# Kernel tuning notes

Hardware: AMD Instinct MI355X
Metric: run time of the kernel (lower is better)

Reference implementation:

```python
import jax, jax.numpy as jnp
import numpy as np

VOCAB, E, H = 32000, 512, 512
B, T = 256, 128
EPS = 1e-12  # F.normalize eps


def setup_inputs() -> dict:
    key = jax.random.key(0)
    ks = jax.random.split(key, 9)
    s_e = 1.0 / np.sqrt(E)
    s_h = 1.0 / np.sqrt(H)
    captions = jax.random.randint(ks[0], (B, T), 0, VOCAB, dtype=jnp.int32)
    emb = jax.random.normal(ks[1], (VOCAB, E), dtype=jnp.float32)
    # fused input->gates weight [E,4H] (gate order: i, f, o, g) and bias [4H]
    Wx = jax.random.uniform(ks[2], (E, 4 * H), jnp.float32, -s_e, s_e)
    bx = jax.random.uniform(ks[3], (4 * H,), jnp.float32, -s_e, s_e)
    # fused hidden->gates weight [H,4H] and bias [4H]
    Uh = jax.random.uniform(ks[4], (H, 4 * H), jnp.float32, -s_h, s_h)
    bu = jax.random.uniform(ks[5], (4 * H,), jnp.float32, -s_h, s_h)
    fcW = jax.random.uniform(ks[6], (H, E), jnp.float32, -s_h, s_h)
    fcb = jax.random.uniform(ks[7], (E,), jnp.float32, -s_h, s_h)
    return {"captions": captions, "emb": emb, "Wx": Wx, "bx": bx,
            "Uh": Uh, "bu": bu, "fcW": fcW, "fcb": fcb}


def reference(captions, emb, Wx, bx, Uh, bu, fcW, fcb):
    # padding_idx=0: embedding row 0 is zero
    emb = emb.at[0].set(0.0)
    x = emb[captions]  # [B,T,E]
    # precompute all input-to-gate projections in one fused GEMM
    xg = jnp.einsum('bte,ef->btf', x, Wx) + bx  # [B,T,4H]

    def step(carry, xg_t):
        h, c = carry
        g = xg_t + h @ Uh + bu  # [B,4H]
        i, f, o, gg = jnp.split(g, 4, axis=-1)
        c = jax.nn.sigmoid(f) * c + jax.nn.sigmoid(i) * jnp.tanh(gg)
        h = jax.nn.sigmoid(o) * jnp.tanh(c)
        return (h, c), None

    h0 = jnp.zeros((captions.shape[0], H), xg.dtype)
    (h, _), _ = jax.lax.scan(step, (h0, h0), jnp.swapaxes(xg, 0, 1))
    out = h @ fcW + fcb  # [B,E]
    norm = jnp.sqrt(jnp.sum(out * out, axis=1, keepdims=True))
    return out / jnp.maximum(norm, EPS)
```

## Files before the change

kernel.cpp:

```cpp
#include <hip/hip_runtime.h>

#define B_ 256
#define T_ 128
#define E_ 512
#define H_ 512
#define NG 2048
#define NB 256
#define NT 512

typedef __attribute__((ext_vector_type(8))) short bf16x8;
typedef __attribute__((ext_vector_type(4))) float f32x4;
typedef unsigned long long u64;

__device__ __forceinline__ short f2bf(float f) {
  union { float f; unsigned u; } x; x.f = f;
  unsigned r = x.u + 0x7FFFu + ((x.u >> 16) & 1u);
  return (short)(r >> 16);
}
__device__ __forceinline__ float bf2f(short s) {
  union { unsigned u; float f; } x;
  x.u = ((unsigned)(unsigned short)s) << 16; return x.f;
}
__device__ __forceinline__ float sigm(float x) { return 1.0f / (1.0f + __expf(-x)); }
__device__ __forceinline__ float tanh_(float x) {
  float cx = fminf(fmaxf(x, -9.f), 9.f);
  float e = __expf(2.f * cx);
  return (e - 1.f) / (e + 1.f);
}

__global__ __launch_bounds__(256) void prep_w(const float* __restrict__ Wx,
                                              const float* __restrict__ Uh,
                                              short* __restrict__ Wt) {
  __shared__ float tile[64][65];
  const int k0 = blockIdx.x * 64;
  const int j0 = blockIdx.y * 64;
  const int tx = threadIdx.x & 63, ty = threadIdx.x >> 6;
#pragma unroll
  for (int r = 0; r < 16; ++r) {
    int k = k0 + r * 4 + ty;
    float v = (k < 512) ? Wx[(size_t)k * NG + j0 + tx]
                        : Uh[(size_t)(k - 512) * NG + j0 + tx];
    tile[r * 4 + ty][tx] = v;
  }
  __syncthreads();
#pragma unroll
  for (int r = 0; r < 16; ++r) {
    int j = j0 + r * 4 + ty;
    Wt[(size_t)j * 1024 + k0 + tx] = f2bf(tile[tx][r * 4 + ty]);
  }
}

__global__ __launch_bounds__(256) void stage_x(const int* __restrict__ captions,
                                               const float* __restrict__ emb,
                                               short* __restrict__ xs) {
  const int bid = blockIdx.x;
  const int t = bid >> 8, b = bid & 255;
  const int tok = captions[b * T_ + t];
  short* o = xs + (size_t)bid * E_;
  const float* src = emb + (size_t)tok * E_;
  int e0 = threadIdx.x, e1 = threadIdx.x + 256;
  if (tok) { o[e0] = f2bf(src[e0]); o[e1] = f2bf(src[e1]); }
  else     { o[e0] = 0;             o[e1] = 0; }
}

__global__ __launch_bounds__(NT, 2) void lstm_all(
    const short* __restrict__ xs,
    const short* __restrict__ Wt,
    const float* __restrict__ bx, const float* __restrict__ bu,
    unsigned* __restrict__ hb0, unsigned* __restrict__ hb1,
    unsigned* __restrict__ flags) {
  __shared__ float part[2][3][2][4][16][20];

  const int tid = threadIdx.x;
  const int wid = tid >> 6, lane = tid & 63;
  const int l15 = lane & 15, l4 = lane >> 4;
  const int kq = wid >> 1, mh = wid & 1;
  const int mg = blockIdx.x >> 5, jt = blockIdx.x & 31;
  const int j0 = jt * 16;
  const int rA = mg * 32 + mh * 16 + l15;

  bf16x8 bfr[4][8];
#pragma unroll
  for (int g = 0; g < 4; ++g) {
    const short* wp = Wt + (size_t)(g * 512 + j0 + l15) * 1024 + kq * 256 + l4 * 8;
#pragma unroll
    for (int ks = 0; ks < 8; ++ks)
      bfr[g][ks] = *(const bf16x8*)(wp + ks * 32);
  }
#pragma unroll
  for (int g = 0; g < 4; ++g)
#pragma unroll
    for (int ks = 0; ks < 8; ++ks)
      asm volatile("" : "+v"(bfr[g][ks]));

  const int J = j0 + l15;
  const float bi  = bx[J] + bu[J];
  const float bf_ = bx[512 + J] + bu[512 + J];
  const float bo  = bx[1024 + J] + bu[1024 + J];
  const float bg  = bx[1536 + J] + bu[1536 + J];
  float c_reg[4] = {0.f, 0.f, 0.f, 0.f};

  unsigned* fl = flags + mg * 64 * 32;

  for (int t = 0; t < T_; ++t) {
    const int tp = t & 1;
    unsigned* hout = tp ? hb1 : hb0;
    const unsigned* hin = tp ? hb0 : hb1;

    f32x4 acc[4] = {{0,0,0,0},{0,0,0,0},{0,0,0,0},{0,0,0,0}};

    if (kq < 2) {
      const short* ab = xs + ((size_t)t * B_ + rA) * E_ + kq * 256 + l4 * 8;
      bf16x8 af[8];
#pragma unroll
      for (int ks = 0; ks < 8; ++ks) af[ks] = *(const bf16x8*)(ab + ks * 32);
#pragma unroll
      for (int ks = 0; ks < 8; ++ks)
#pragma unroll
        for (int g = 0; g < 4; ++g)
          acc[g] = __builtin_amdgcn_mfma_f32_16x16x32_bf16(af[ks], bfr[g][ks], acc[g], 0, 0, 0);
    } else if (t > 0) {
      const unsigned* myfl = fl + (mh * 32 + (kq - 2) * 16 + l15) * 32;
      unsigned v = __hip_atomic_load(myfl, __ATOMIC_RELAXED, __HIP_MEMORY_SCOPE_AGENT);
      while (!__all((int)(v >= (unsigned)t))) {
        __builtin_amdgcn_s_sleep(1);
        v = __hip_atomic_load(myfl, __ATOMIC_RELAXED, __HIP_MEMORY_SCOPE_AGENT);
      }
      asm volatile("" ::: "memory");
      const u64* hp = (const u64*)hin + (size_t)rA * 128 + (kq - 2) * 64 + l4 * 2;
      u64 w[16];
#pragma unroll
      for (int ks = 0; ks < 8; ++ks) {
        w[ks * 2]     = __hip_atomic_load(hp + ks * 8,     __ATOMIC_RELAXED, __HIP_MEMORY_SCOPE_AGENT);
        w[ks * 2 + 1] = __hip_atomic_load(hp + ks * 8 + 1, __ATOMIC_RELAXED, __HIP_MEMORY_SCOPE_AGENT);
      }
#pragma unroll
      for (int ks = 0; ks < 8; ++ks) {
        union { bf16x8 v; unsigned u[4]; } fa;
        fa.u[0] = (unsigned)w[ks * 2];
        fa.u[1] = (unsigned)(w[ks * 2] >> 32);
        fa.u[2] = (unsigned)w[ks * 2 + 1];
        fa.u[3] = (unsigned)(w[ks * 2 + 1] >> 32);
#pragma unroll
        for (int g = 0; g < 4; ++g)
          acc[g] = __builtin_amdgcn_mfma_f32_16x16x32_bf16(fa.v, bfr[g][ks], acc[g], 0, 0, 0);
      }
    }

    if (kq != 2) {
      const int slot = (kq == 3) ? 2 : kq;
#pragma unroll
      for (int g = 0; g < 4; ++g)
#pragma unroll
        for (int r = 0; r < 4; ++r)
          part[tp][slot][mh][g][l4 * 4 + r][l15] = acc[g][r];
    }
    asm volatile("s_waitcnt lgkmcnt(0)" ::: "memory");
    __builtin_amdgcn_s_barrier();

    if (kq == 2) {
#pragma unroll
      for (int g = 0; g < 4; ++g)
#pragma unroll
        for (int r = 0; r < 4; ++r)
          acc[g][r] += part[tp][0][mh][g][l4 * 4 + r][l15]
                     + part[tp][1][mh][g][l4 * 4 + r][l15]
                     + part[tp][2][mh][g][l4 * 4 + r][l15];
      unsigned hw[4];
#pragma unroll
      for (int r = 0; r < 4; ++r) {
        float iv = acc[0][r] + bi, fv = acc[1][r] + bf_;
        float ov = acc[2][r] + bo, gv = acc[3][r] + bg;
        float cn = sigm(fv) * c_reg[r] + sigm(iv) * tanh_(gv);
        c_reg[r] = cn;
        hw[r] = (unsigned)(unsigned short)f2bf(sigm(ov) * tanh_(cn));
      }
#pragma unroll
      for (int r = 0; r < 4; ++r) {
        unsigned other = (unsigned)__shfl_xor((int)hw[r], 1, 64);
        if (!(l15 & 1)) {
          const int R = mg * 32 + mh * 16 + l4 * 4 + r;
          __hip_atomic_store(hout + (size_t)R * 256 + (J >> 1),
                             hw[r] | (other << 16),
                             __ATOMIC_RELAXED, __HIP_MEMORY_SCOPE_AGENT);
        }
      }
      asm volatile("s_waitcnt vmcnt(0)" ::: "memory");
      if (lane == 0)
        __hip_atomic_store(fl + (mh * 32 + jt) * 32, (unsigned)(t + 1),
                           __ATOMIC_RELAXED, __HIP_MEMORY_SCOPE_AGENT);
    }
  }
}

__global__ __launch_bounds__(256) void final_fc(const unsigned* __restrict__ h,
                                                const float* __restrict__ fcW,
                                                const float* __restrict__ fcb,
                                                float* __restrict__ out) {
  const int b = blockIdx.x, tid = threadIdx.x;
  __shared__ float hrow[512];
  __shared__ float red[256];
  {
    unsigned w = h[(size_t)b * 256 + tid];
    hrow[tid * 2]     = bf2f((short)(w & 0xFFFF));
    hrow[tid * 2 + 1] = bf2f((short)(w >> 16));
  }
  __syncthreads();
  float a0 = fcb[tid], a1 = fcb[tid + 256];
  for (int k = 0; k < 512; ++k) {
    float hv = hrow[k];
    a0 += hv * fcW[(size_t)k * 512 + tid];
    a1 += hv * fcW[(size_t)k * 512 + tid + 256];
  }
  red[tid] = a0 * a0 + a1 * a1;
  __syncthreads();
  for (int s = 128; s > 0; s >>= 1) {
    if (tid < s) red[tid] += red[tid + s];
    __syncthreads();
  }
  float scale = 1.0f / fmaxf(sqrtf(red[0]), 1e-12f);
  out[(size_t)b * 512 + tid] = a0 * scale;
  out[(size_t)b * 512 + tid + 256] = a1 * scale;
}

extern "C" void kernel_launch(void* const* d_in, const int* in_sizes, int n_in,
                              void* d_out, int out_size, void* d_ws, size_t ws_size,
                              hipStream_t stream) {
  const int*   captions = (const int*)d_in[0];
  const float* emb      = (const float*)d_in[1];
  const float* Wx       = (const float*)d_in[2];
  const float* bx       = (const float*)d_in[3];
  const float* Uh       = (const float*)d_in[4];
  const float* bu       = (const float*)d_in[5];
  const float* fcW      = (const float*)d_in[6];
  const float* fcb      = (const float*)d_in[7];
  float* out = (float*)d_out;

  char* ws = (char*)d_ws;
  size_t off = 0;
  auto alloc = [&](size_t bytes) {
    char* p = ws + off;
    off += (bytes + 255) & ~(size_t)255;
    return p;
  };
  short*    Wt    = (short*)alloc((size_t)NG * 1024 * 2);
  short*    xs    = (short*)alloc((size_t)T_ * B_ * E_ * 2);
  unsigned* hb0   = (unsigned*)alloc((size_t)B_ * 256 * 4);
  unsigned* hb1   = (unsigned*)alloc((size_t)B_ * 256 * 4);
  unsigned* flags = (unsigned*)alloc(8 * 64 * 32 * 4);

  hipMemsetAsync(flags, 0, 8 * 64 * 32 * 4, stream);

  prep_w<<<dim3(16, 32), 256, 0, stream>>>(Wx, Uh, Wt);
  stage_x<<<T_ * B_, 256, 0, stream>>>(captions, emb, xs);

  void* kargs[] = {(void*)&xs, (void*)&Wt, (void*)&bx, (void*)&bu,
                   (void*)&hb0, (void*)&hb1, (void*)&flags};
  hipLaunchCooperativeKernel((const void*)lstm_all, dim3(NB), dim3(NT),
                             kargs, 0, stream);

  final_fc<<<B_, 256, 0, stream>>>(hb1, fcW, fcb, out);
}
```

Before: 695.0 us.

## Split recurrent h wait into halves and vectorize LDS partial-sum exchange

The recurrent-path waves now wait only on the flags of the producers of the first half of the K range, run those MFMAs, and then wait for the rest. This overlaps part of the cross-block synchronisation with compute. The spin loop backs off to longer sleeps after a few tries, and the shared-memory partial sums become f32x4 stores and loads in place of scalar accesses. The risks are finer-grained polling overhead, added wake-up latency from the longer sleep, and possible LDS bank conflicts now that the padding is gone.

```diff
diff --git a/kernel.cpp b/kernel.cpp
--- a/kernel.cpp
+++ b/kernel.cpp
@@ -69,7 +69,7 @@
     const float* __restrict__ bx, const float* __restrict__ bu,
     unsigned* __restrict__ hb0, unsigned* __restrict__ hb1,
     unsigned* __restrict__ flags) {
-  __shared__ float part[2][3][2][4][16][20];
+  __shared__ f32x4 part[2][3][2][4][4][16];
 
   const int tid = threadIdx.x;
   const int wid = tid >> 6, lane = tid & 63;
@@ -120,22 +120,25 @@
         for (int g = 0; g < 4; ++g)
           acc[g] = __builtin_amdgcn_mfma_f32_16x16x32_bf16(af[ks], bfr[g][ks], acc[g], 0, 0, 0);
     } else if (t > 0) {
+      const unsigned thr = (unsigned)t;
       const unsigned* myfl = fl + (mh * 32 + (kq - 2) * 16 + l15) * 32;
+      const u64* hp = (const u64*)hin + (size_t)rA * 128 + (kq - 2) * 64 + l4 * 2;
       unsigned v = __hip_atomic_load(myfl, __ATOMIC_RELAXED, __HIP_MEMORY_SCOPE_AGENT);
-      while (!__all((int)(v >= (unsigned)t))) {
-        __builtin_amdgcn_s_sleep(1);
+      int spin = 0;
+      while (!__all((int)((l15 >= 8) | (v >= thr)))) {
+        if (spin++ < 4) __builtin_amdgcn_s_sleep(1);
+        else            __builtin_amdgcn_s_sleep(8);
         v = __hip_atomic_load(myfl, __ATOMIC_RELAXED, __HIP_MEMORY_SCOPE_AGENT);
       }
       asm volatile("" ::: "memory");
-      const u64* hp = (const u64*)hin + (size_t)rA * 128 + (kq - 2) * 64 + l4 * 2;
       u64 w[16];
 #pragma unroll
-      for (int ks = 0; ks < 8; ++ks) {
+      for (int ks = 0; ks < 4; ++ks) {
         w[ks * 2]     = __hip_atomic_load(hp + ks * 8,     __ATOMIC_RELAXED, __HIP_MEMORY_SCOPE_AGENT);
         w[ks * 2 + 1] = __hip_atomic_load(hp + ks * 8 + 1, __ATOMIC_RELAXED, __HIP_MEMORY_SCOPE_AGENT);
       }
 #pragma unroll
-      for (int ks = 0; ks < 8; ++ks) {
+      for (int ks = 0; ks < 4; ++ks) {
         union { bf16x8 v; unsigned u[4]; } fa;
         fa.u[0] = (unsigned)w[ks * 2];
         fa.u[1] = (unsigned)(w[ks * 2] >> 32);
@@ -145,15 +148,35 @@
         for (int g = 0; g < 4; ++g)
           acc[g] = __builtin_amdgcn_mfma_f32_16x16x32_bf16(fa.v, bfr[g][ks], acc[g], 0, 0, 0);
       }
+      while (!__all((int)(v >= thr))) {
+        if (spin++ < 4) __builtin_amdgcn_s_sleep(1);
+        else            __builtin_amdgcn_s_sleep(8);
+        v = __hip_atomic_load(myfl, __ATOMIC_RELAXED, __HIP_MEMORY_SCOPE_AGENT);
+      }
+      asm volatile("" ::: "memory");
+#pragma unroll
+      for (int ks = 4; ks < 8; ++ks) {
+        w[ks * 2]     = __hip_atomic_load(hp + ks * 8,     __ATOMIC_RELAXED, __HIP_MEMORY_SCOPE_AGENT);
+        w[ks * 2 + 1] = __hip_atomic_load(hp + ks * 8 + 1, __ATOMIC_RELAXED, __HIP_MEMORY_SCOPE_AGENT);
+      }
+#pragma unroll
+      for (int ks = 4; ks < 8; ++ks) {
+        union { bf16x8 v; unsigned u[4]; } fa;
+        fa.u[0] = (unsigned)w[ks * 2];
+        fa.u[1] = (unsigned)(w[ks * 2] >> 32);
+        fa.u[2] = (unsigned)w[ks * 2 + 1];
+        fa.u[3] = (unsigned)(w[ks * 2 + 1] >> 32);
+#pragma unroll
+        for (int g = 0; g < 4; ++g)
+          acc[g] = __builtin_amdgcn_mfma_f32_16x16x32_bf16(fa.v, bfr[g][ks], acc[g], 0, 0, 0);
+      }
     }
 
     if (kq != 2) {
       const int slot = (kq == 3) ? 2 : kq;
 #pragma unroll
       for (int g = 0; g < 4; ++g)
-#pragma unroll
-        for (int r = 0; r < 4; ++r)
-          part[tp][slot][mh][g][l4 * 4 + r][l15] = acc[g][r];
+        part[tp][slot][mh][g][l4][l15] = acc[g];
     }
     asm volatile("s_waitcnt lgkmcnt(0)" ::: "memory");
     __builtin_amdgcn_s_barrier();
@@ -161,11 +184,9 @@
     if (kq == 2) {
 #pragma unroll
       for (int g = 0; g < 4; ++g)
-#pragma unroll
-        for (int r = 0; r < 4; ++r)
-          acc[g][r] += part[tp][0][mh][g][l4 * 4 + r][l15]
-                     + part[tp][1][mh][g][l4 * 4 + r][l15]
-                     + part[tp][2][mh][g][l4 * 4 + r][l15];
+        acc[g] += part[tp][0][mh][g][l4][l15]
+                + part[tp][1][mh][g][l4][l15]
+                + part[tp][2][mh][g][l4][l15];
       unsigned hw[4];
 #pragma unroll
       for (int r = 0; r < 4; ++r) {
```

Measured after the change: 694.6 us. Within noise of the previous version (-0.1%).

## Split gate reduction and cell update across input-side waves, add per-publisher flags

Applied to the files above, without the earlier changes.

The cross-wave reduction of gate partial sums and the LSTM cell update move from the two h-side waves to the two x-side waves (kq<2). Each wave now finishes 2 rows instead of 4, and all four waves write f32x4 partials to shared memory. Flags are split per (kq, mh) publisher, and consumers poll the matching publisher flags. The spin-wait also backs off to a longer sleep after a few tries. The intent is to take the nonlinear update off the h-path waves so they can start polling for the next step sooner, and to spread the elementwise work wider. The cost is extra shared-memory traffic and longer sleeps, which can add wake-up latency.

```diff
diff --git a/kernel.cpp b/kernel.cpp
--- a/kernel.cpp
+++ b/kernel.cpp
@@ -69,7 +69,7 @@
     const float* __restrict__ bx, const float* __restrict__ bu,
     unsigned* __restrict__ hb0, unsigned* __restrict__ hb1,
     unsigned* __restrict__ flags) {
-  __shared__ float part[2][3][2][4][16][20];
+  __shared__ f32x4 part[2][4][2][4][4][16];
 
   const int tid = threadIdx.x;
   const int wid = tid >> 6, lane = tid & 63;
@@ -98,9 +98,9 @@
   const float bf_ = bx[512 + J] + bu[512 + J];
   const float bo  = bx[1024 + J] + bu[1024 + J];
   const float bg  = bx[1536 + J] + bu[1536 + J];
-  float c_reg[4] = {0.f, 0.f, 0.f, 0.f};
-
-  unsigned* fl = flags + mg * 64 * 32;
+  float c_reg[2] = {0.f, 0.f};
+
+  unsigned* fl = flags + mg * 4 * 32 * 32;
 
   for (int t = 0; t < T_; ++t) {
     const int tp = t & 1;
@@ -120,10 +120,15 @@
         for (int g = 0; g < 4; ++g)
           acc[g] = __builtin_amdgcn_mfma_f32_16x16x32_bf16(af[ks], bfr[g][ks], acc[g], 0, 0, 0);
     } else if (t > 0) {
-      const unsigned* myfl = fl + (mh * 32 + (kq - 2) * 16 + l15) * 32;
+      const unsigned thr = (unsigned)t;
+      const int jtp = (lane & 15) + (kq - 2) * 16;
+      const int pub = ((lane >> 4) & 1) * 2 + mh;
+      const unsigned* myfl = fl + (pub * 32 + jtp) * 32;
       unsigned v = __hip_atomic_load(myfl, __ATOMIC_RELAXED, __HIP_MEMORY_SCOPE_AGENT);
-      while (!__all((int)(v >= (unsigned)t))) {
-        __builtin_amdgcn_s_sleep(1);
+      int spin = 0;
+      while (!__all((int)(v >= thr))) {
+        if (spin++ < 4) __builtin_amdgcn_s_sleep(1);
+        else            __builtin_amdgcn_s_sleep(8);
         v = __hip_atomic_load(myfl, __ATOMIC_RELAXED, __HIP_MEMORY_SCOPE_AGENT);
       }
       asm volatile("" ::: "memory");
@@ -147,39 +152,36 @@
       }
     }
 
-    if (kq != 2) {
-      const int slot = (kq == 3) ? 2 : kq;
-#pragma unroll
-      for (int g = 0; g < 4; ++g)
-#pragma unroll
-        for (int r = 0; r < 4; ++r)
-          part[tp][slot][mh][g][l4 * 4 + r][l15] = acc[g][r];
-    }
+#pragma unroll
+    for (int g = 0; g < 4; ++g)
+      part[tp][kq][mh][g][l4][l15] = acc[g];
     asm volatile("s_waitcnt lgkmcnt(0)" ::: "memory");
     __builtin_amdgcn_s_barrier();
 
-    if (kq == 2) {
-#pragma unroll
-      for (int g = 0; g < 4; ++g)
-#pragma unroll
-        for (int r = 0; r < 4; ++r)
-          acc[g][r] += part[tp][0][mh][g][l4 * 4 + r][l15]
-                     + part[tp][1][mh][g][l4 * 4 + r][l15]
-                     + part[tp][2][mh][g][l4 * 4 + r][l15];
-      unsigned hw[4];
-#pragma unroll
-      for (int r = 0; r < 4; ++r) {
-        float iv = acc[0][r] + bi, fv = acc[1][r] + bf_;
-        float ov = acc[2][r] + bo, gv = acc[3][r] + bg;
+    if (kq < 2) {
+      unsigned hw[2];
+#pragma unroll
+      for (int r = 0; r < 2; ++r) {
+        const int Rm = kq * 8 + l4 * 2 + r;
+        const int ri = Rm >> 2, rc = Rm & 3;
+        float sums[4];
+#pragma unroll
+        for (int g = 0; g < 4; ++g)
+          sums[g] = part[tp][0][mh][g][ri][l15][rc]
+                  + part[tp][1][mh][g][ri][l15][rc]
+                  + part[tp][2][mh][g][ri][l15][rc]
+                  + part[tp][3][mh][g][ri][l15][rc];
+        float iv = sums[0] + bi, fv = sums[1] + bf_;
+        float ov = sums[2] + bo, gv = sums[3] + bg;
         float cn = sigm(fv) * c_reg[r] + sigm(iv) * tanh_(gv);
         c_reg[r] = cn;
         hw[r] = (unsigned)(unsigned short)f2bf(sigm(ov) * tanh_(cn));
       }
 #pragma unroll
-      for (int r = 0; r < 4; ++r) {
+      for (int r = 0; r < 2; ++r) {
         unsigned other = (unsigned)__shfl_xor((int)hw[r], 1, 64);
         if (!(l15 & 1)) {
-          const int R = mg * 32 + mh * 16 + l4 * 4 + r;
+          const int R = mg * 32 + mh * 16 + kq * 8 + l4 * 2 + r;
           __hip_atomic_store(hout + (size_t)R * 256 + (J >> 1),
                              hw[r] | (other << 16),
                              __ATOMIC_RELAXED, __HIP_MEMORY_SCOPE_AGENT);
@@ -187,7 +189,7 @@
       }
       asm volatile("s_waitcnt vmcnt(0)" ::: "memory");
       if (lane == 0)
-        __hip_atomic_store(fl + (mh * 32 + jt) * 32, (unsigned)(t + 1),
+        __hip_atomic_store(fl + ((kq * 2 + mh) * 32 + jt) * 32, (unsigned)(t + 1),
                            __ATOMIC_RELAXED, __HIP_MEMORY_SCOPE_AGENT);
     }
   }
@@ -247,9 +249,9 @@
   short*    xs    = (short*)alloc((size_t)T_ * B_ * E_ * 2);
   unsigned* hb0   = (unsigned*)alloc((size_t)B_ * 256 * 4);
   unsigned* hb1   = (unsigned*)alloc((size_t)B_ * 256 * 4);
-  unsigned* flags = (unsigned*)alloc(8 * 64 * 32 * 4);
-
-  hipMemsetAsync(flags, 0, 8 * 64 * 32 * 4, stream);
+  unsigned* flags = (unsigned*)alloc(8 * 4 * 32 * 32 * 4);
+
+  hipMemsetAsync(flags, 0, 8 * 4 * 32 * 32 * 4, stream);
 
   prep_w<<<dim3(16, 32), 256, 0, stream>>>(Wx, Uh, Wt);
   stage_x<<<T_ * B_, 256, 0, stream>>>(captions, emb, xs);
```

New measurement: 753.9 us. +8.5%, slower.

## Repartition LSTM blocks into 16-row batch groups with 32 hidden columns each

Applied to the files above, without the earlier changes.

Changes the cooperative LSTM decomposition from 8 batch groups of 32 rows by 32 column tiles to 16 batch groups of 16 rows by 16 column tiles of 32 hidden units. Each block's two wave halves now split hidden columns instead of batch rows. A block therefore waits on flags from only 16 other blocks per group rather than 32, which shrinks the cross-block synchronisation fan-in each step. It also stores partial sums as f32x4 vectors in shared memory and adds a backoff to the spin-wait sleep, which may add latency when the wait runs long.

```diff
diff --git a/kernel.cpp b/kernel.cpp
--- a/kernel.cpp
+++ b/kernel.cpp
@@ -69,20 +69,21 @@
     const float* __restrict__ bx, const float* __restrict__ bu,
     unsigned* __restrict__ hb0, unsigned* __restrict__ hb1,
     unsigned* __restrict__ flags) {
-  __shared__ float part[2][3][2][4][16][20];
+  __shared__ f32x4 part[2][3][2][4][4][16];
 
   const int tid = threadIdx.x;
   const int wid = tid >> 6, lane = tid & 63;
   const int l15 = lane & 15, l4 = lane >> 4;
-  const int kq = wid >> 1, mh = wid & 1;
-  const int mg = blockIdx.x >> 5, jt = blockIdx.x & 31;
-  const int j0 = jt * 16;
-  const int rA = mg * 32 + mh * 16 + l15;
+  const int kq = wid >> 1, jh = wid & 1;
+  const int mg = blockIdx.x >> 4, jt = blockIdx.x & 15;
+  const int j0 = jt * 32;
+  const int rA = mg * 16 + l15;
 
   bf16x8 bfr[4][8];
 #pragma unroll
   for (int g = 0; g < 4; ++g) {
-    const short* wp = Wt + (size_t)(g * 512 + j0 + l15) * 1024 + kq * 256 + l4 * 8;
+    const short* wp = Wt + (size_t)(g * 512 + j0 + jh * 16 + l15) * 1024
+                         + kq * 256 + l4 * 8;
 #pragma unroll
     for (int ks = 0; ks < 8; ++ks)
       bfr[g][ks] = *(const bf16x8*)(wp + ks * 32);
@@ -93,14 +94,14 @@
     for (int ks = 0; ks < 8; ++ks)
       asm volatile("" : "+v"(bfr[g][ks]));
 
-  const int J = j0 + l15;
+  const int J = j0 + jh * 16 + l15;
   const float bi  = bx[J] + bu[J];
   const float bf_ = bx[512 + J] + bu[512 + J];
   const float bo  = bx[1024 + J] + bu[1024 + J];
   const float bg  = bx[1536 + J] + bu[1536 + J];
   float c_reg[4] = {0.f, 0.f, 0.f, 0.f};
 
-  unsigned* fl = flags + mg * 64 * 32;
+  unsigned* fl = flags + mg * 1024;
 
   for (int t = 0; t < T_; ++t) {
     const int tp = t & 1;
@@ -120,10 +121,15 @@
         for (int g = 0; g < 4; ++g)
           acc[g] = __builtin_amdgcn_mfma_f32_16x16x32_bf16(af[ks], bfr[g][ks], acc[g], 0, 0, 0);
     } else if (t > 0) {
-      const unsigned* myfl = fl + (mh * 32 + (kq - 2) * 16 + l15) * 32;
+      const unsigned thr = (unsigned)t;
+      const int jtp = (kq - 2) * 8 + (lane >> 1 & 7);
+      const int jhp = lane & 1;
+      const unsigned* myfl = fl + (jhp * 16 + jtp) * 32;
       unsigned v = __hip_atomic_load(myfl, __ATOMIC_RELAXED, __HIP_MEMORY_SCOPE_AGENT);
-      while (!__all((int)(v >= (unsigned)t))) {
-        __builtin_amdgcn_s_sleep(1);
+      int spin = 0;
+      while (!__all((int)((lane >= 16) | (v >= thr)))) {
+        if (spin++ < 4) __builtin_amdgcn_s_sleep(1);
+        else            __builtin_amdgcn_s_sleep(8);
         v = __hip_atomic_load(myfl, __ATOMIC_RELAXED, __HIP_MEMORY_SCOPE_AGENT);
       }
       asm volatile("" ::: "memory");
@@ -151,9 +157,7 @@
       const int slot = (kq == 3) ? 2 : kq;
 #pragma unroll
       for (int g = 0; g < 4; ++g)
-#pragma unroll
-        for (int r = 0; r < 4; ++r)
-          part[tp][slot][mh][g][l4 * 4 + r][l15] = acc[g][r];
+        part[tp][slot][jh][g][l4][l15] = acc[g];
     }
     asm volatile("s_waitcnt lgkmcnt(0)" ::: "memory");
     __builtin_amdgcn_s_barrier();
@@ -161,11 +165,9 @@
     if (kq == 2) {
 #pragma unroll
       for (int g = 0; g < 4; ++g)
-#pragma unroll
-        for (int r = 0; r < 4; ++r)
-          acc[g][r] += part[tp][0][mh][g][l4 * 4 + r][l15]
-                     + part[tp][1][mh][g][l4 * 4 + r][l15]
-                     + part[tp][2][mh][g][l4 * 4 + r][l15];
+        acc[g] += part[tp][0][jh][g][l4][l15]
+                + part[tp][1][jh][g][l4][l15]
+                + part[tp][2][jh][g][l4][l15];
       unsigned hw[4];
 #pragma unroll
       for (int r = 0; r < 4; ++r) {
@@ -179,7 +181,7 @@
       for (int r = 0; r < 4; ++r) {
         unsigned other = (unsigned)__shfl_xor((int)hw[r], 1, 64);
         if (!(l15 & 1)) {
-          const int R = mg * 32 + mh * 16 + l4 * 4 + r;
+          const int R = mg * 16 + l4 * 4 + r;
           __hip_atomic_store(hout + (size_t)R * 256 + (J >> 1),
                              hw[r] | (other << 16),
                              __ATOMIC_RELAXED, __HIP_MEMORY_SCOPE_AGENT);
@@ -187,7 +189,7 @@
       }
       asm volatile("s_waitcnt vmcnt(0)" ::: "memory");
       if (lane == 0)
-        __hip_atomic_store(fl + (mh * 32 + jt) * 32, (unsigned)(t + 1),
+        __hip_atomic_store(fl + (jh * 16 + jt) * 32, (unsigned)(t + 1),
                            __ATOMIC_RELAXED, __HIP_MEMORY_SCOPE_AGENT);
     }
   }
@@ -247,9 +249,9 @@
   short*    xs    = (short*)alloc((size_t)T_ * B_ * E_ * 2);
   unsigned* hb0   = (unsigned*)alloc((size_t)B_ * 256 * 4);
   unsigned* hb1   = (unsigned*)alloc((size_t)B_ * 256 * 4);
-  unsigned* flags = (unsigned*)alloc(8 * 64 * 32 * 4);
-
-  hipMemsetAsync(flags, 0, 8 * 64 * 32 * 4, stream);
+  unsigned* flags = (unsigned*)alloc(16 * 2 * 16 * 32 * 4);
+
+  hipMemsetAsync(flags, 0, 16 * 2 * 16 * 32 * 4, stream);
 
   prep_w<<<dim3(16, 32), 256, 0, stream>>>(Wx, Uh, Wt);
   stage_x<<<T_ * B_, 256, 0, stream>>>(captions, emb, xs);
```

New measurement: 685.8 us. About the same (-1.3%).
